# Kernel optimization log

Hardware: AMD Instinct MI355X
Metric: run time of the kernel (lower is better)

## Reference

```python
import math
import jax, jax.numpy as jnp
import numpy as np

D = 512
MEM_LEN = 1024
RATIO = 2


def setup_inputs() -> dict:
    key = jax.random.key(0)
    ks = jax.random.split(key, 16)
    s = 1.0 / math.sqrt(D)
    inp = {
        "x": jax.random.normal(ks[0], (4, 2048, D), jnp.float32),
        "fine_mem": jax.random.normal(ks[1], (8, 256, D), jnp.float32),
        "cmem_seq": jax.random.normal(ks[2], (16, 128, D), jnp.float32),
        "comp_query": jax.random.normal(ks[3], (D,), jnp.float32) * 0.02,
        "comp_W": jax.random.normal(ks[4], (D, D), jnp.float32) * s,
        "comp_b": jnp.zeros((D,), jnp.float32),
        "k_W": jax.random.normal(ks[5], (D, D), jnp.float32) * s,
        "k_b": jnp.zeros((D,), jnp.float32),
        "v_W": jax.random.normal(ks[6], (D, D), jnp.float32) * s,
        "v_b": jnp.zeros((D,), jnp.float32),
        "xk_W": jax.random.normal(ks[7], (D, D), jnp.float32) * s,
        "xk_b": jnp.zeros((D,), jnp.float32),
        "ck_W": jax.random.normal(ks[8], (D, D), jnp.float32) * s,
        "ck_b": jnp.zeros((D,), jnp.float32),
        "cv_W": jax.random.normal(ks[9], (D, D), jnp.float32) * s,
        "cv_b": jnp.zeros((D,), jnp.float32),
    }
    return inp


def _compress(combined, comp_query, comp_W, comp_b):
    # AttentionPoolCompressor, vectorized: L tokens -> L//RATIO pooled tokens
    L, d = combined.shape
    L_out = max(L // RATIO, 1)
    c = combined.reshape(L_out, RATIO, d)                      # [L_out, r, d]
    logits = jnp.einsum("d,lrd->lr", comp_query, c) * (d ** -0.5)
    w = jax.nn.softmax(logits, axis=-1)
    pooled = jnp.einsum("lr,lrd->ld", w, c)                    # [L_out, d]
    return pooled @ comp_W + comp_b


def _interp_linear(comp, L):
    # F.interpolate(mode='linear', align_corners=False) along length dim
    L_out = comp.shape[0]
    i = jnp.arange(L, dtype=jnp.float32)
    src = jnp.clip((i + 0.5) * (L_out / L) - 0.5, 0.0, L_out - 1)
    i0 = jnp.floor(src).astype(jnp.int32)
    i1 = jnp.minimum(i0 + 1, L_out - 1)
    frac = (src - i0)[:, None]
    return (1.0 - frac) * comp[i0] + frac * comp[i1]


def reference(x, fine_mem, cmem_seq, comp_query, comp_W, comp_b,
              k_W, k_b, v_W, v_b, xk_W, xk_b, ck_W, ck_b, cv_W, cv_b):
    B, S, d = x.shape
    Nf, Lm, _ = fine_mem.shape
    scale = d ** -0.5

    # keys/values over the ORIGINAL memories (projections precede eviction)
    fine_k = fine_mem @ k_W + k_b      # [Nf, Lm, d]
    fine_v = fine_mem @ v_W + v_b
    cmem_k = cmem_seq @ ck_W + ck_b    # [Nc, Lc, d]
    cmem_v = cmem_seq @ cv_W + cv_b

    # eviction: take leading chunks until cumsum >= mem_len/2 (static)
    K = min(int(math.ceil(0.5 * MEM_LEN / Lm)), Nf)
    combined = fine_mem[:K].reshape(K * Lm, d)                 # [L, d]
    compressed = _compress(combined, comp_query, comp_W, comp_b)
    decoded = _interp_linear(compressed, combined.shape[0])
    recon_loss = jnp.mean((decoded - combined) ** 2)

    # cross-attention over concatenated memory
    query = x @ xk_W + xk_b                                    # [B, S, d]
    mem_k = jnp.concatenate([fine_k.reshape(-1, d), cmem_k.reshape(-1, d)], 0)
    mem_v = jnp.concatenate([fine_v.reshape(-1, d), cmem_v.reshape(-1, d)], 0)
    scores = jnp.einsum("bsd,md->bsm", query, mem_k) * scale   # [B, S, M]
    attn = jax.nn.softmax(scores, axis=-1)
    mem_out = jnp.einsum("bsm,md->bsd", attn, mem_v)
    output = x + mem_out
    return (output, recon_loss)
```

## Files before the change

kernel.cpp:

```cpp
#include <hip/hip_runtime.h>

typedef __attribute__((ext_vector_type(8))) short bf16x8;
typedef __attribute__((ext_vector_type(4))) float f32x4;

#define MFMA16(a,b,c) __builtin_amdgcn_mfma_f32_16x16x32_bf16((a),(b),(c),0,0,0)

__device__ __forceinline__ unsigned short f2bf(float f) {
  unsigned int u = __builtin_bit_cast(unsigned int, f);
  u = (u + 0x7FFFu + ((u >> 16) & 1u)) >> 16;
  return (unsigned short)u;
}
__device__ __forceinline__ float bf2f(unsigned short u) {
  unsigned int v = ((unsigned int)u) << 16;
  return __builtin_bit_cast(float, v);
}
__device__ __forceinline__ unsigned int pack_bf16(float a, float b) {
  return ((unsigned int)f2bf(b) << 16) | (unsigned int)f2bf(a);
}

__global__ __launch_bounds__(256) void cvt_bf16_all(
    const float* __restrict__ x, const float* __restrict__ fine,
    const float* __restrict__ cmem, unsigned short* __restrict__ abf)
{
  size_t off = ((size_t)blockIdx.x * 256 + threadIdx.x) * 4;
  const float* src;
  if (off < (size_t)8192*512)        src = x + off;
  else if (off < (size_t)10240*512)  src = fine + (off - (size_t)8192*512);
  else                               src = cmem + (off - (size_t)10240*512);
  float4 v = *(const float4*)src;
  unsigned long long pk = (unsigned long long)f2bf(v.x)
    | ((unsigned long long)f2bf(v.y) << 16)
    | ((unsigned long long)f2bf(v.z) << 32)
    | ((unsigned long long)f2bf(v.w) << 48);
  *(unsigned long long*)(abf + off) = pk;
}

__global__ __launch_bounds__(256) void wt_transpose5(
    const float* __restrict__ W0, const float* __restrict__ W1,
    const float* __restrict__ W2, const float* __restrict__ W3,
    const float* __restrict__ W4,
    unsigned short* __restrict__ O0, unsigned short* __restrict__ O1,
    unsigned short* __restrict__ O2, unsigned short* __restrict__ O3,
    unsigned short* __restrict__ O4)
{
  const float* W; unsigned short* Wt;
  switch (blockIdx.z) {
    case 0: W = W0; Wt = O0; break;
    case 1: W = W1; Wt = O1; break;
    case 2: W = W2; Wt = O2; break;
    case 3: W = W3; Wt = O3; break;
    default: W = W4; Wt = O4; break;
  }
  __shared__ unsigned short T[32][33];
  int kb = blockIdx.x * 32, nb = blockIdx.y * 32;
  int tx = threadIdx.x & 31, ty = threadIdx.x >> 5;
  #pragma unroll
  for (int s = 0; s < 4; ++s)
    T[ty + 8*s][tx] = f2bf(W[(kb + ty + 8*s)*512 + nb + tx]);
  __syncthreads();
  #pragma unroll
  for (int s = 0; s < 4; ++s)
    Wt[(nb + ty + 8*s)*512 + kb + tx] = T[tx][ty + 8*s];
}

__global__ __launch_bounds__(256) void v_transpose(const unsigned short* __restrict__ V,
    unsigned short* __restrict__ Vt)
{
  __shared__ unsigned short T[32][33];
  int mb = blockIdx.x * 32, db = blockIdx.y * 32;
  int tx = threadIdx.x & 31, ty = threadIdx.x >> 5;
  #pragma unroll
  for (int s = 0; s < 4; ++s)
    T[ty + 8*s][tx] = V[(mb + ty + 8*s)*512 + db + tx];
  __syncthreads();
  #pragma unroll
  for (int s = 0; s < 4; ++s)
    Vt[(db + ty + 8*s)*4096 + mb + tx] = T[tx][ty + 8*s];
}

__global__ __launch_bounds__(256) void proj_all(
    const unsigned short* __restrict__ abf,
    const unsigned short* __restrict__ WtXK, const unsigned short* __restrict__ WtK,
    const unsigned short* __restrict__ WtV,  const unsigned short* __restrict__ WtCK,
    const unsigned short* __restrict__ WtCV,
    const float* __restrict__ xkb, const float* __restrict__ kb2, const float* __restrict__ vb2,
    const float* __restrict__ ckb, const float* __restrict__ cvb,
    unsigned short* __restrict__ qry, unsigned short* __restrict__ memk,
    unsigned short* __restrict__ memv)
{
  const unsigned short* A; const unsigned short* Bt; const float* bias; unsigned short* C;
  int m0;
  int bx = blockIdx.x;
  if (bx < 64) { A = abf; Bt = WtXK; bias = xkb; C = qry; m0 = bx * 128; }
  else {
    int seg = (bx - 64) >> 4;
    m0 = ((bx - 64) & 15) * 128;
    switch (seg) {
      case 0:  A = abf + (size_t)8192*512;  Bt = WtK;  bias = kb2; C = memk;            break;
      case 1:  A = abf + (size_t)10240*512; Bt = WtCK; bias = ckb; C = memk + 2048*512; break;
      case 2:  A = abf + (size_t)8192*512;  Bt = WtV;  bias = vb2; C = memv;            break;
      default: A = abf + (size_t)10240*512; Bt = WtCV; bias = cvb; C = memv + 2048*512; break;
    }
  }
  const float cs = (bx < 64) ? 0.04419417382415922f : 1.0f;

  __shared__ unsigned short As[128*32];
  __shared__ unsigned short Bs[64*32];
  const int tid = threadIdx.x;
  const int w = tid >> 6, lane = tid & 63;
  const int lr = lane & 15, lg = lane >> 4;
  const int wm = w >> 1, wn = w & 1;
  const int n0 = blockIdx.y * 64;

  f32x4 acc[4][2];
  #pragma unroll
  for (int mt = 0; mt < 4; ++mt)
    #pragma unroll
    for (int nt = 0; nt < 2; ++nt) acc[mt][nt] = (f32x4){0.f,0.f,0.f,0.f};

  const int arow = lane >> 2;
  const int acol = (lane & 3) * 8;

  for (int kb = 0; kb < 512; kb += 32) {
    #pragma unroll
    for (int j = 0; j < 2; ++j) {
      int r0 = (w*2 + j) * 16;
      __builtin_amdgcn_global_load_lds(
        (const __attribute__((address_space(1))) unsigned int*)
          (A + (size_t)(m0 + r0 + arow)*512 + kb + acol),
        (__attribute__((address_space(3))) unsigned int*)(&As[r0*32]), 16, 0, 0);
    }
    {
      int r0 = w * 16;
      __builtin_amdgcn_global_load_lds(
        (const __attribute__((address_space(1))) unsigned int*)
          (Bt + (size_t)(n0 + r0 + arow)*512 + kb + acol),
        (__attribute__((address_space(3))) unsigned int*)(&Bs[r0*32]), 16, 0, 0);
    }
    __syncthreads();
    bf16x8 af[4], bfr[2];
    #pragma unroll
    for (int mt = 0; mt < 4; ++mt)
      af[mt] = *(const bf16x8*)&As[(wm*64 + mt*16 + lr)*32 + lg*8];
    #pragma unroll
    for (int nt = 0; nt < 2; ++nt)
      bfr[nt] = *(const bf16x8*)&Bs[(wn*32 + nt*16 + lr)*32 + lg*8];
    #pragma unroll
    for (int mt = 0; mt < 4; ++mt)
      #pragma unroll
      for (int nt = 0; nt < 2; ++nt)
        acc[mt][nt] = MFMA16(af[mt], bfr[nt], acc[mt][nt]);
    __syncthreads();
  }
  #pragma unroll
  for (int nt = 0; nt < 2; ++nt) {
    int col = n0 + wn*32 + nt*16 + lr;
    float bv = bias[col];
    #pragma unroll
    for (int mt = 0; mt < 4; ++mt) {
      #pragma unroll
      for (int j = 0; j < 4; ++j) {
        int row = m0 + wm*64 + mt*16 + lg*4 + j;
        C[row*512 + col] = f2bf((acc[mt][nt][j] + bv) * cs);
      }
    }
  }
}

template<int NC>
__global__ __launch_bounds__(256, 2) void attn_kernel(
    const unsigned short* __restrict__ q,
    const unsigned short* __restrict__ mk,
    const unsigned short* __restrict__ vt,
    unsigned short* __restrict__ opart,
    float* __restrict__ mpart,
    float* __restrict__ lpart)
{
  constexpr int CK = 4096 / NC;
  constexpr int ITERS = CK / 64;
  constexpr int PLW = 68;

  __shared__ unsigned short Ks[64*520];
  __shared__ unsigned short Pl[64*PLW];
  __shared__ float Fl[64];
  __shared__ unsigned int Tf[4];

  const int tid = threadIdx.x;
  const int w = tid >> 6, lane = tid & 63;
  const int lr = lane & 15, lg = lane >> 4;
  const int bid = blockIdx.x;
  const int chunk = bid & (NC - 1);
  const int qb = bid / NC;
  const int q0blk = qb * 64;
  const int kvbase = chunk * CK;

  const unsigned short* qgp = q + (size_t)(q0blk + w*16 + lr) * 512 + lg*8;

  f32x4 o[32];
  #pragma unroll
  for (int nt = 0; nt < 32; ++nt) o[nt] = (f32x4){0.f,0.f,0.f,0.f};
  float m = -1e30f, l = 0.f;

  const unsigned short* vgp = vt + (size_t)(w*128 + lr) * 4096 + kvbase + lg*8;

  #define STAGE_K(IT) do {                                                        \
    int kv0_ = kvbase + (IT) * 64;                                                \
    _Pragma("unroll")                                                             \
    for (int i_ = 0; i_ < 16; ++i_) {                                             \
      int r_ = w * 16 + i_;                                                       \
      __builtin_amdgcn_global_load_lds(                                           \
        (const __attribute__((address_space(1))) unsigned int*)                   \
          (mk + (kv0_ + r_)*512 + lane*8),                                        \
        (__attribute__((address_space(3))) unsigned int*)(&Ks[r_*520]), 16, 0, 0);\
    }                                                                             \
  } while (0)

  STAGE_K(0);
  __syncthreads();

  const unsigned short* kp = &Ks[lr * 520];

  for (int it = 0; it < ITERS; ++it) {
    f32x4 t0 = (f32x4){0.f,0.f,0.f,0.f}, t1 = (f32x4){0.f,0.f,0.f,0.f};
    f32x4 t2 = (f32x4){0.f,0.f,0.f,0.f}, t3 = (f32x4){0.f,0.f,0.f,0.f};
    __builtin_amdgcn_s_setprio(1);
    #pragma unroll
    for (int ks = 0; ks < 16; ++ks) {
      bf16x8 qf  = *(const bf16x8*)(qgp + ks*32);
      bf16x8 kb0 = *(const bf16x8*)(kp + ks*32 + lg*8);
      bf16x8 kb1 = *(const bf16x8*)(kp + 16*520 + ks*32 + lg*8);
      bf16x8 kb2 = *(const bf16x8*)(kp + 32*520 + ks*32 + lg*8);
      bf16x8 kb3 = *(const bf16x8*)(kp + 48*520 + ks*32 + lg*8);
      t0 = MFMA16(kb0, qf, t0);
      t1 = MFMA16(kb1, qf, t1);
      t2 = MFMA16(kb2, qf, t2);
      t3 = MFMA16(kb3, qf, t3);
    }
    __builtin_amdgcn_s_setprio(0);

    float pm = fmaxf(fmaxf(fmaxf(t0[0], t0[1]), fmaxf(t0[2], t0[3])),
                     fmaxf(fmaxf(t1[0], t1[1]), fmaxf(t1[2], t1[3])));
    pm = fmaxf(pm, fmaxf(fmaxf(fmaxf(t2[0], t2[1]), fmaxf(t2[2], t2[3])),
                         fmaxf(fmaxf(t3[0], t3[1]), fmaxf(t3[2], t3[3]))));
    pm = fmaxf(pm, __shfl_xor(pm, 16));
    pm = fmaxf(pm, __shfl_xor(pm, 32));

    bool trig = !__all(pm <= m + 8.f);
    if (trig) {
      float mn = fmaxf(m, pm);
      float fl = __expf(m - mn);
      l *= fl;
      m = mn;
      if (lg == 0) Fl[w*16 + lr] = fl;
    }
    if (lane == 0) Tf[w] = trig ? 1u : 0u;

    float p0[4], p1[4], p2[4], p3[4];
    #pragma unroll
    for (int j = 0; j < 4; ++j) {
      p0[j] = __expf(t0[j] - m);
      p1[j] = __expf(t1[j] - m);
      p2[j] = __expf(t2[j] - m);
      p3[j] = __expf(t3[j] - m);
    }
    float rs = ((p0[0]+p0[1]) + (p0[2]+p0[3])) + ((p1[0]+p1[1]) + (p1[2]+p1[3]))
             + ((p2[0]+p2[1]) + (p2[2]+p2[3])) + ((p3[0]+p3[1]) + (p3[2]+p3[3]));
    rs += __shfl_xor(rs, 16);
    rs += __shfl_xor(rs, 32);
    l += rs;

    {
      unsigned short* pr = &Pl[(w*16 + lr)*PLW + lg*4];
      *(uint2*)(pr)      = make_uint2(pack_bf16(p0[0], p0[1]), pack_bf16(p0[2], p0[3]));
      *(uint2*)(pr + 16) = make_uint2(pack_bf16(p1[0], p1[1]), pack_bf16(p1[2], p1[3]));
      *(uint2*)(pr + 32) = make_uint2(pack_bf16(p2[0], p2[1]), pack_bf16(p2[2], p2[3]));
      *(uint2*)(pr + 48) = make_uint2(pack_bf16(p3[0], p3[1]), pack_bf16(p3[2], p3[3]));
    }
    __syncthreads();

    if (it + 1 < ITERS) STAGE_K(it + 1);

    unsigned int tf0 = Tf[0], tf1 = Tf[1], tf2 = Tf[2], tf3 = Tf[3];
    if (tf0 | tf1 | tf2 | tf3) {
      #pragma unroll
      for (int qt = 0; qt < 4; ++qt) {
        unsigned int tfq = (qt == 0) ? tf0 : (qt == 1) ? tf1 : (qt == 2) ? tf2 : tf3;
        if (tfq) {
          f32x4 fq = *(const f32x4*)&Fl[qt*16 + lg*4];
          #pragma unroll
          for (int dt = 0; dt < 8; ++dt) {
            o[qt*8 + dt][0] *= fq[0]; o[qt*8 + dt][1] *= fq[1];
            o[qt*8 + dt][2] *= fq[2]; o[qt*8 + dt][3] *= fq[3];
          }
        }
      }
    }

    const unsigned short* vit = vgp + it*64;
    #pragma unroll
    for (int kvh = 0; kvh < 2; ++kvh) {
      bf16x8 pa[4];
      #pragma unroll
      for (int qt = 0; qt < 4; ++qt)
        pa[qt] = *(const bf16x8*)&Pl[(qt*16 + lr)*PLW + kvh*32 + lg*8];
      #pragma unroll
      for (int dh = 0; dh < 2; ++dh) {
        bf16x8 vb[4];
        #pragma unroll
        for (int dt = 0; dt < 4; ++dt)
          vb[dt] = *(const bf16x8*)(vit + kvh*32 + (size_t)(dh*4 + dt)*16*4096);
        __builtin_amdgcn_s_setprio(1);
        #pragma unroll
        for (int qt = 0; qt < 4; ++qt) {
          #pragma unroll
          for (int dt = 0; dt < 4; ++dt)
            o[qt*8 + dh*4 + dt] = MFMA16(pa[qt], vb[dt], o[qt*8 + dh*4 + dt]);
        }
        __builtin_amdgcn_s_setprio(0);
      }
    }
    __syncthreads();
  }

  unsigned short* ob = opart + (size_t)chunk * 8192 * 512;
  #pragma unroll
  for (int qt = 0; qt < 4; ++qt) {
    #pragma unroll
    for (int dt = 0; dt < 8; ++dt) {
      #pragma unroll
      for (int j = 0; j < 4; ++j) {
        int row = q0blk + qt*16 + lg*4 + j;
        int col = w*128 + dt*16 + lr;
        ob[row*512 + col] = f2bf(o[qt*8 + dt][j]);
      }
    }
  }
  if (lane < 16) {
    mpart[chunk*8192 + q0blk + w*16 + lane] = m;
    lpart[chunk*8192 + q0blk + w*16 + lane] = l;
  }
  #undef STAGE_K
}

template<int NC>
__global__ __launch_bounds__(256) void attn_combine(
    const unsigned short* __restrict__ opart, const float* __restrict__ mpart,
    const float* __restrict__ lpart, const float* __restrict__ x,
    float* __restrict__ out)
{
  int row = blockIdx.x * 4 + (threadIdx.x >> 6);
  int t = threadIdx.x & 63;
  int d0 = t * 8;
  float mc[NC], lc[NC];
  #pragma unroll
  for (int c = 0; c < NC; ++c) { mc[c] = mpart[c*8192 + row]; lc[c] = lpart[c*8192 + row]; }
  float M = mc[0];
  #pragma unroll
  for (int c = 1; c < NC; ++c) M = fmaxf(M, mc[c]);
  float wc[NC], denom = 0.f;
  #pragma unroll
  for (int c = 0; c < NC; ++c) { wc[c] = __expf(mc[c] - M); denom += wc[c] * lc[c]; }
  float inv = 1.0f / denom;
  float acc[8] = {0.f,0.f,0.f,0.f,0.f,0.f,0.f,0.f};
  const unsigned short* base = opart + (size_t)row*512 + d0;
  #pragma unroll
  for (int c = 0; c < NC; ++c) {
    int4 v = *(const int4*)(base + (size_t)c * 8192 * 512);
    const unsigned short* u = (const unsigned short*)&v;
    #pragma unroll
    for (int e = 0; e < 8; ++e) acc[e] += wc[c] * bf2f(u[e]);
  }
  float4 xv0 = *(const float4*)(x + row*512 + d0);
  float4 xv1 = *(const float4*)(x + row*512 + d0 + 4);
  float4 o0, o1;
  o0.x = xv0.x + acc[0]*inv; o0.y = xv0.y + acc[1]*inv;
  o0.z = xv0.z + acc[2]*inv; o0.w = xv0.w + acc[3]*inv;
  o1.x = xv1.x + acc[4]*inv; o1.y = xv1.y + acc[5]*inv;
  o1.z = xv1.z + acc[6]*inv; o1.w = xv1.w + acc[7]*inv;
  *(float4*)(out + row*512 + d0)     = o0;
  *(float4*)(out + row*512 + d0 + 4) = o1;
}

__global__ __launch_bounds__(256) void compress_pool(const float* __restrict__ fine,
    const float* __restrict__ cq, float* __restrict__ pooled, float* __restrict__ loss)
{
  if (blockIdx.x == 0 && threadIdx.x == 0) *loss = 0.f;
  int l = blockIdx.x;
  int t = threadIdx.x;
  const float* c0 = fine + (2*l)*512;
  const float* c1 = c0 + 512;
  float q0 = cq[t], q1 = cq[t+256];
  float a0 = q0*c0[t] + q1*c0[t+256];
  float a1 = q0*c1[t] + q1*c1[t+256];
  #pragma unroll
  for (int m = 1; m < 64; m <<= 1) { a0 += __shfl_xor(a0, m); a1 += __shfl_xor(a1, m); }
  __shared__ float r0[4], r1[4];
  int w = t >> 6;
  if ((t & 63) == 0) { r0[w] = a0; r1[w] = a1; }
  __syncthreads();
  const float sc = 0.04419417382415922f;
  float g0 = (r0[0]+r0[1]+r0[2]+r0[3]) * sc;
  float g1 = (r1[0]+r1[1]+r1[2]+r1[3]) * sc;
  float mx = fmaxf(g0, g1);
  float e0 = __expf(g0-mx), e1 = __expf(g1-mx);
  float inv = 1.0f/(e0+e1);
  float w0 = e0*inv, w1 = e1*inv;
  pooled[l*512 + t]       = w0*c0[t]     + w1*c1[t];
  pooled[l*512 + t + 256] = w0*c0[t+256] + w1*c1[t+256];
}

__global__ __launch_bounds__(256) void comp_gemm(const float* __restrict__ P,
    const float* __restrict__ W, const float* __restrict__ b, float* __restrict__ out)
{
  int gid = blockIdx.x * 256 + threadIdx.x;
  int m = gid >> 9, n = gid & 511;
  const float* a = P + m * 512;
  float acc = b[n];
  #pragma unroll 8
  for (int k = 0; k < 512; ++k) acc += a[k] * W[k*512 + n];
  out[gid] = acc;
}

__global__ __launch_bounds__(256) void interp_loss(const float* __restrict__ comp,
    const float* __restrict__ fine, float* __restrict__ loss)
{
  float acc = 0.f;
  #pragma unroll
  for (int s = 0; s < 4; ++s) {
    int e = blockIdx.x*1024 + s*256 + threadIdx.x;
    int i = e >> 9, d = e & 511;
    float src = fminf(fmaxf((i + 0.5f)*0.5f - 0.5f, 0.f), 255.f);
    int i0 = (int)src;
    int i1 = min(i0 + 1, 255);
    float fr = src - (float)i0;
    float dec = (1.f - fr)*comp[i0*512 + d] + fr*comp[i1*512 + d];
    float df = dec - fine[e];
    acc += df*df;
  }
  #pragma unroll
  for (int m = 1; m < 64; m <<= 1) acc += __shfl_xor(acc, m);
  __shared__ float r[4];
  int w = threadIdx.x >> 6;
  if ((threadIdx.x & 63) == 0) r[w] = acc;
  __syncthreads();
  if (threadIdx.x == 0)
    atomicAdd(loss, (r[0]+r[1]+r[2]+r[3]) * (1.0f/262144.0f));
}

extern "C" void kernel_launch(void* const* d_in, const int* in_sizes, int n_in,
                              void* d_out, int out_size, void* d_ws, size_t ws_size,
                              hipStream_t stream) {
  const float* x     = (const float*)d_in[0];
  const float* fine  = (const float*)d_in[1];
  const float* cmem  = (const float*)d_in[2];
  const float* cq    = (const float*)d_in[3];
  const float* compW = (const float*)d_in[4];
  const float* compb = (const float*)d_in[5];
  const float* kW    = (const float*)d_in[6];
  const float* kb_   = (const float*)d_in[7];
  const float* vW    = (const float*)d_in[8];
  const float* vb_   = (const float*)d_in[9];
  const float* xkW   = (const float*)d_in[10];
  const float* xkb   = (const float*)d_in[11];
  const float* ckW   = (const float*)d_in[12];
  const float* ckb   = (const float*)d_in[13];
  const float* cvW   = (const float*)d_in[14];
  const float* cvb   = (const float*)d_in[15];

  char* ws = (char*)d_ws;
  const size_t WT = 512*512*2;
  unsigned short* WtK  = (unsigned short*)(ws + 0*WT);
  unsigned short* WtV  = (unsigned short*)(ws + 1*WT);
  unsigned short* WtCK = (unsigned short*)(ws + 2*WT);
  unsigned short* WtCV = (unsigned short*)(ws + 3*WT);
  unsigned short* WtXK = (unsigned short*)(ws + 4*WT);
  char* base = ws + 5*WT;
  unsigned short* memk = (unsigned short*)(base);
  unsigned short* memv = (unsigned short*)(base + (4u<<20));
  unsigned short* vt   = (unsigned short*)(base + (8u<<20));
  unsigned short* qry  = (unsigned short*)(base + (12u<<20));
  float* pooled        = (float*)(base + (20u<<20));
  float* comp          = (float*)(base + (20u<<20) + (512u<<10));
  unsigned short* opart= (unsigned short*)(base + (21u<<20));
  float* mpart         = (float*)(base + (21u<<20) + (32ull<<20));
  float* lpart         = mpart + 4*8192;
  unsigned short* abf  = (unsigned short*)(base + (54u<<20));

  float* out  = (float*)d_out;
  float* loss = out + 8192*512;

  cvt_bf16_all<<<6144, 256, 0, stream>>>(x, fine, cmem, abf);

  wt_transpose5<<<dim3(16,16,5), 256, 0, stream>>>(kW, vW, ckW, cvW, xkW,
                                                   WtK, WtV, WtCK, WtCV, WtXK);

  proj_all<<<dim3(128,8), 256, 0, stream>>>(abf,
      WtXK, WtK, WtV, WtCK, WtCV,
      xkb, kb_, vb_, ckb, cvb,
      qry, memk, memv);

  v_transpose<<<dim3(128,16), 256, 0, stream>>>(memv, vt);

  attn_kernel<4><<<512, 256, 0, stream>>>(qry, memk, vt, opart, mpart, lpart);
  attn_combine<4><<<2048, 256, 0, stream>>>(opart, mpart, lpart, x, out);

  compress_pool<<<256, 256, 0, stream>>>(fine, cq, pooled, loss);
  comp_gemm<<<512, 256, 0, stream>>>(pooled, compW, compb, comp);
  interp_loss<<<256, 256, 0, stream>>>(comp, fine, loss);
}
```

Measured before the change: 186.7 us.

## Merge independent kernels into fewer launches and drop setprio in attention

Groups the original nine launches into five. Bf16 conversion, weight transposes and compress pooling now share one prep kernel. The projection GEMM and compression GEMM share one kernel, and the V transpose and interp-loss share a post kernel, with each branch picked by block index. The goal is to cut launch overhead and let the small recon-loss work overlap with the big stages instead of running serially at the end. It also removes the s_setprio hints around the MFMA loops in the attention kernel, which may change wave scheduling.

```diff
diff --git a/kernel.cpp b/kernel.cpp
--- a/kernel.cpp
+++ b/kernel.cpp
@@ -18,67 +18,80 @@
   return ((unsigned int)f2bf(b) << 16) | (unsigned int)f2bf(a);
 }
 
-__global__ __launch_bounds__(256) void cvt_bf16_all(
+__global__ __launch_bounds__(256) void prep_kernel(
     const float* __restrict__ x, const float* __restrict__ fine,
-    const float* __restrict__ cmem, unsigned short* __restrict__ abf)
-{
-  size_t off = ((size_t)blockIdx.x * 256 + threadIdx.x) * 4;
-  const float* src;
-  if (off < (size_t)8192*512)        src = x + off;
-  else if (off < (size_t)10240*512)  src = fine + (off - (size_t)8192*512);
-  else                               src = cmem + (off - (size_t)10240*512);
-  float4 v = *(const float4*)src;
-  unsigned long long pk = (unsigned long long)f2bf(v.x)
-    | ((unsigned long long)f2bf(v.y) << 16)
-    | ((unsigned long long)f2bf(v.z) << 32)
-    | ((unsigned long long)f2bf(v.w) << 48);
-  *(unsigned long long*)(abf + off) = pk;
-}
-
-__global__ __launch_bounds__(256) void wt_transpose5(
+    const float* __restrict__ cmem, unsigned short* __restrict__ abf,
     const float* __restrict__ W0, const float* __restrict__ W1,
     const float* __restrict__ W2, const float* __restrict__ W3,
     const float* __restrict__ W4,
     unsigned short* __restrict__ O0, unsigned short* __restrict__ O1,
     unsigned short* __restrict__ O2, unsigned short* __restrict__ O3,
-    unsigned short* __restrict__ O4)
-{
-  const float* W; unsigned short* Wt;
-  switch (blockIdx.z) {
-    case 0: W = W0; Wt = O0; break;
-    case 1: W = W1; Wt = O1; break;
-    case 2: W = W2; Wt = O2; break;
-    case 3: W = W3; Wt = O3; break;
-    default: W = W4; Wt = O4; break;
-  }
-  __shared__ unsigned short T[32][33];
-  int kb = blockIdx.x * 32, nb = blockIdx.y * 32;
-  int tx = threadIdx.x & 31, ty = threadIdx.x >> 5;
-  #pragma unroll
-  for (int s = 0; s < 4; ++s)
-    T[ty + 8*s][tx] = f2bf(W[(kb + ty + 8*s)*512 + nb + tx]);
-  __syncthreads();
-  #pragma unroll
-  for (int s = 0; s < 4; ++s)
-    Wt[(nb + ty + 8*s)*512 + kb + tx] = T[tx][ty + 8*s];
-}
-
-__global__ __launch_bounds__(256) void v_transpose(const unsigned short* __restrict__ V,
-    unsigned short* __restrict__ Vt)
+    unsigned short* __restrict__ O4,
+    const float* __restrict__ cq, float* __restrict__ pooled, float* __restrict__ loss)
 {
   __shared__ unsigned short T[32][33];
-  int mb = blockIdx.x * 32, db = blockIdx.y * 32;
-  int tx = threadIdx.x & 31, ty = threadIdx.x >> 5;
-  #pragma unroll
-  for (int s = 0; s < 4; ++s)
-    T[ty + 8*s][tx] = V[(mb + ty + 8*s)*512 + db + tx];
-  __syncthreads();
-  #pragma unroll
-  for (int s = 0; s < 4; ++s)
-    Vt[(db + ty + 8*s)*4096 + mb + tx] = T[tx][ty + 8*s];
-}
-
-__global__ __launch_bounds__(256) void proj_all(
+  __shared__ float r0s[4], r1s[4];
+  int bx = blockIdx.x;
+  int tid = threadIdx.x;
+
+  if (bx < 6144) {
+    size_t off = ((size_t)bx * 256 + tid) * 4;
+    const float* src;
+    if (off < (size_t)8192*512)        src = x + off;
+    else if (off < (size_t)10240*512)  src = fine + (off - (size_t)8192*512);
+    else                               src = cmem + (off - (size_t)10240*512);
+    float4 v = *(const float4*)src;
+    unsigned long long pk = (unsigned long long)f2bf(v.x)
+      | ((unsigned long long)f2bf(v.y) << 16)
+      | ((unsigned long long)f2bf(v.z) << 32)
+      | ((unsigned long long)f2bf(v.w) << 48);
+    *(unsigned long long*)(abf + off) = pk;
+  } else if (bx < 7424) {
+    int idx = bx - 6144;
+    int z = idx >> 8, rem = idx & 255;
+    int kb = (rem & 15) * 32, nb = (rem >> 4) * 32;
+    const float* W; unsigned short* Wt;
+    switch (z) {
+      case 0: W = W0; Wt = O0; break;
+      case 1: W = W1; Wt = O1; break;
+      case 2: W = W2; Wt = O2; break;
+      case 3: W = W3; Wt = O3; break;
+      default: W = W4; Wt = O4; break;
+    }
+    int tx = tid & 31, ty = tid >> 5;
+    #pragma unroll
+    for (int s = 0; s < 4; ++s)
+      T[ty + 8*s][tx] = f2bf(W[(kb + ty + 8*s)*512 + nb + tx]);
+    __syncthreads();
+    #pragma unroll
+    for (int s = 0; s < 4; ++s)
+      Wt[(nb + ty + 8*s)*512 + kb + tx] = T[tx][ty + 8*s];
+  } else {
+    int l = bx - 7424;
+    if (l == 0 && tid == 0) *loss = 0.f;
+    const float* c0 = fine + (2*l)*512;
+    const float* c1 = c0 + 512;
+    float q0 = cq[tid], q1 = cq[tid+256];
+    float a0 = q0*c0[tid] + q1*c0[tid+256];
+    float a1 = q0*c1[tid] + q1*c1[tid+256];
+    #pragma unroll
+    for (int mm = 1; mm < 64; mm <<= 1) { a0 += __shfl_xor(a0, mm); a1 += __shfl_xor(a1, mm); }
+    int w = tid >> 6;
+    if ((tid & 63) == 0) { r0s[w] = a0; r1s[w] = a1; }
+    __syncthreads();
+    const float sc = 0.04419417382415922f;
+    float g0 = (r0s[0]+r0s[1]+r0s[2]+r0s[3]) * sc;
+    float g1 = (r1s[0]+r1s[1]+r1s[2]+r1s[3]) * sc;
+    float mx = fmaxf(g0, g1);
+    float e0 = __expf(g0-mx), e1 = __expf(g1-mx);
+    float inv = 1.0f/(e0+e1);
+    float w0 = e0*inv, w1 = e1*inv;
+    pooled[l*512 + tid]       = w0*c0[tid]     + w1*c1[tid];
+    pooled[l*512 + tid + 256] = w0*c0[tid+256] + w1*c1[tid+256];
+  }
+}
+
+__global__ __launch_bounds__(256) void gemm_kernel(
     const unsigned short* __restrict__ abf,
     const unsigned short* __restrict__ WtXK, const unsigned short* __restrict__ WtK,
     const unsigned short* __restrict__ WtV,  const unsigned short* __restrict__ WtCK,
@@ -86,11 +99,30 @@
     const float* __restrict__ xkb, const float* __restrict__ kb2, const float* __restrict__ vb2,
     const float* __restrict__ ckb, const float* __restrict__ cvb,
     unsigned short* __restrict__ qry, unsigned short* __restrict__ memk,
-    unsigned short* __restrict__ memv)
+    unsigned short* __restrict__ memv,
+    const float* __restrict__ P, const float* __restrict__ compW,
+    const float* __restrict__ compb, float* __restrict__ comp)
 {
+  __shared__ unsigned short As[128*32];
+  __shared__ unsigned short Bs[64*32];
+  const int tid = threadIdx.x;
+  int bxg = blockIdx.x;
+
+  if (bxg >= 1024) {
+    int gid = (bxg - 1024) * 256 + tid;
+    int m = gid >> 9, n = gid & 511;
+    const float* a = P + m * 512;
+    float acc = compb[n];
+    #pragma unroll 8
+    for (int k = 0; k < 512; ++k) acc += a[k] * compW[k*512 + n];
+    comp[gid] = acc;
+    return;
+  }
+
+  int bx = bxg >> 3;
+  int n0 = (bxg & 7) * 64;
   const unsigned short* A; const unsigned short* Bt; const float* bias; unsigned short* C;
   int m0;
-  int bx = blockIdx.x;
   if (bx < 64) { A = abf; Bt = WtXK; bias = xkb; C = qry; m0 = bx * 128; }
   else {
     int seg = (bx - 64) >> 4;
@@ -104,13 +136,9 @@
   }
   const float cs = (bx < 64) ? 0.04419417382415922f : 1.0f;
 
-  __shared__ unsigned short As[128*32];
-  __shared__ unsigned short Bs[64*32];
-  const int tid = threadIdx.x;
   const int w = tid >> 6, lane = tid & 63;
   const int lr = lane & 15, lg = lane >> 4;
   const int wm = w >> 1, wn = w & 1;
-  const int n0 = blockIdx.y * 64;
 
   f32x4 acc[4][2];
   #pragma unroll
@@ -164,6 +192,51 @@
         C[row*512 + col] = f2bf((acc[mt][nt][j] + bv) * cs);
       }
     }
+  }
+}
+
+__global__ __launch_bounds__(256) void post_kernel(
+    const unsigned short* __restrict__ V, unsigned short* __restrict__ Vt,
+    const float* __restrict__ comp, const float* __restrict__ fine,
+    float* __restrict__ loss)
+{
+  __shared__ unsigned short T[32][33];
+  __shared__ float r[4];
+  int bx = blockIdx.x;
+  int tid = threadIdx.x;
+
+  if (bx < 2048) {
+    int mb = (bx & 127) * 32, db = (bx >> 7) * 32;
+    int tx = tid & 31, ty = tid >> 5;
+    #pragma unroll
+    for (int s = 0; s < 4; ++s)
+      T[ty + 8*s][tx] = V[(mb + ty + 8*s)*512 + db + tx];
+    __syncthreads();
+    #pragma unroll
+    for (int s = 0; s < 4; ++s)
+      Vt[(db + ty + 8*s)*4096 + mb + tx] = T[tx][ty + 8*s];
+  } else {
+    int bid = bx - 2048;
+    float acc = 0.f;
+    #pragma unroll
+    for (int s = 0; s < 4; ++s) {
+      int e = bid*1024 + s*256 + tid;
+      int i = e >> 9, d = e & 511;
+      float src = fminf(fmaxf((i + 0.5f)*0.5f - 0.5f, 0.f), 255.f);
+      int i0 = (int)src;
+      int i1 = min(i0 + 1, 255);
+      float fr = src - (float)i0;
+      float dec = (1.f - fr)*comp[i0*512 + d] + fr*comp[i1*512 + d];
+      float df = dec - fine[e];
+      acc += df*df;
+    }
+    #pragma unroll
+    for (int mm = 1; mm < 64; mm <<= 1) acc += __shfl_xor(acc, mm);
+    int w = tid >> 6;
+    if ((tid & 63) == 0) r[w] = acc;
+    __syncthreads();
+    if (tid == 0)
+      atomicAdd(loss, (r[0]+r[1]+r[2]+r[3]) * (1.0f/262144.0f));
   }
 }
 
@@ -223,7 +296,6 @@
   for (int it = 0; it < ITERS; ++it) {
     f32x4 t0 = (f32x4){0.f,0.f,0.f,0.f}, t1 = (f32x4){0.f,0.f,0.f,0.f};
     f32x4 t2 = (f32x4){0.f,0.f,0.f,0.f}, t3 = (f32x4){0.f,0.f,0.f,0.f};
-    __builtin_amdgcn_s_setprio(1);
     #pragma unroll
     for (int ks = 0; ks < 16; ++ks) {
       bf16x8 qf  = *(const bf16x8*)(qgp + ks*32);
@@ -236,7 +308,6 @@
       t2 = MFMA16(kb2, qf, t2);
       t3 = MFMA16(kb3, qf, t3);
     }
-    __builtin_amdgcn_s_setprio(0);
 
     float pm = fmaxf(fmaxf(fmaxf(t0[0], t0[1]), fmaxf(t0[2], t0[3])),
                      fmaxf(fmaxf(t1[0], t1[1]), fmaxf(t1[2], t1[3])));
@@ -309,14 +380,12 @@
         #pragma unroll
         for (int dt = 0; dt < 4; ++dt)
           vb[dt] = *(const bf16x8*)(vit + kvh*32 + (size_t)(dh*4 + dt)*16*4096);
-        __builtin_amdgcn_s_setprio(1);
         #pragma unroll
         for (int qt = 0; qt < 4; ++qt) {
           #pragma unroll
           for (int dt = 0; dt < 4; ++dt)
             o[qt*8 + dh*4 + dt] = MFMA16(pa[qt], vb[dt], o[qt*8 + dh*4 + dt]);
         }
-        __builtin_amdgcn_s_setprio(0);
       }
     }
     __syncthreads();
@@ -379,72 +448,6 @@
   o1.z = xv1.z + acc[6]*inv; o1.w = xv1.w + acc[7]*inv;
   *(float4*)(out + row*512 + d0)     = o0;
   *(float4*)(out + row*512 + d0 + 4) = o1;
-}
-
-__global__ __launch_bounds__(256) void compress_pool(const float* __restrict__ fine,
-    const float* __restrict__ cq, float* __restrict__ pooled, float* __restrict__ loss)
-{
-  if (blockIdx.x == 0 && threadIdx.x == 0) *loss = 0.f;
-  int l = blockIdx.x;
-  int t = threadIdx.x;
-  const float* c0 = fine + (2*l)*512;
-  const float* c1 = c0 + 512;
-  float q0 = cq[t], q1 = cq[t+256];
-  float a0 = q0*c0[t] + q1*c0[t+256];
-  float a1 = q0*c1[t] + q1*c1[t+256];
-  #pragma unroll
-  for (int m = 1; m < 64; m <<= 1) { a0 += __shfl_xor(a0, m); a1 += __shfl_xor(a1, m); }
-  __shared__ float r0[4], r1[4];
-  int w = t >> 6;
-  if ((t & 63) == 0) { r0[w] = a0; r1[w] = a1; }
-  __syncthreads();
-  const float sc = 0.04419417382415922f;
-  float g0 = (r0[0]+r0[1]+r0[2]+r0[3]) * sc;
-  float g1 = (r1[0]+r1[1]+r1[2]+r1[3]) * sc;
-  float mx = fmaxf(g0, g1);
-  float e0 = __expf(g0-mx), e1 = __expf(g1-mx);
-  float inv = 1.0f/(e0+e1);
-  float w0 = e0*inv, w1 = e1*inv;
-  pooled[l*512 + t]       = w0*c0[t]     + w1*c1[t];
-  pooled[l*512 + t + 256] = w0*c0[t+256] + w1*c1[t+256];
-}
-
-__global__ __launch_bounds__(256) void comp_gemm(const float* __restrict__ P,
-    const float* __restrict__ W, const float* __restrict__ b, float* __restrict__ out)
-{
-  int gid = blockIdx.x * 256 + threadIdx.x;
-  int m = gid >> 9, n = gid & 511;
-  const float* a = P + m * 512;
-  float acc = b[n];
-  #pragma unroll 8
-  for (int k = 0; k < 512; ++k) acc += a[k] * W[k*512 + n];
-  out[gid] = acc;
-}
-
-__global__ __launch_bounds__(256) void interp_loss(const float* __restrict__ comp,
-    const float* __restrict__ fine, float* __restrict__ loss)
-{
-  float acc = 0.f;
-  #pragma unroll
-  for (int s = 0; s < 4; ++s) {
-    int e = blockIdx.x*1024 + s*256 + threadIdx.x;
-    int i = e >> 9, d = e & 511;
-    float src = fminf(fmaxf((i + 0.5f)*0.5f - 0.5f, 0.f), 255.f);
-    int i0 = (int)src;
-    int i1 = min(i0 + 1, 255);
-    float fr = src - (float)i0;
-    float dec = (1.f - fr)*comp[i0*512 + d] + fr*comp[i1*512 + d];
-    float df = dec - fine[e];
-    acc += df*df;
-  }
-  #pragma unroll
-  for (int m = 1; m < 64; m <<= 1) acc += __shfl_xor(acc, m);
-  __shared__ float r[4];
-  int w = threadIdx.x >> 6;
-  if ((threadIdx.x & 63) == 0) r[w] = acc;
-  __syncthreads();
-  if (threadIdx.x == 0)
-    atomicAdd(loss, (r[0]+r[1]+r[2]+r[3]) * (1.0f/262144.0f));
 }
 
 extern "C" void kernel_launch(void* const* d_in, const int* in_sizes, int n_in,
@@ -489,22 +492,18 @@
   float* out  = (float*)d_out;
   float* loss = out + 8192*512;
 
-  cvt_bf16_all<<<6144, 256, 0, stream>>>(x, fine, cmem, abf);
-
-  wt_transpose5<<<dim3(16,16,5), 256, 0, stream>>>(kW, vW, ckW, cvW, xkW,
-                                                   WtK, WtV, WtCK, WtCV, WtXK);
-
-  proj_all<<<dim3(128,8), 256, 0, stream>>>(abf,
+  prep_kernel<<<7680, 256, 0, stream>>>(x, fine, cmem, abf,
+      kW, vW, ckW, cvW, xkW, WtK, WtV, WtCK, WtCV, WtXK,
+      cq, pooled, loss);
+
+  gemm_kernel<<<1536, 256, 0, stream>>>(abf,
       WtXK, WtK, WtV, WtCK, WtCV,
       xkb, kb_, vb_, ckb, cvb,
-      qry, memk, memv);
-
-  v_transpose<<<dim3(128,16), 256, 0, stream>>>(memv, vt);
+      qry, memk, memv,
+      pooled, compW, compb, comp);
+
+  post_kernel<<<2304, 256, 0, stream>>>(memv, vt, comp, fine, loss);
 
   attn_kernel<4><<<512, 256, 0, stream>>>(qry, memk, vt, opart, mpart, lpart);
   attn_combine<4><<<2048, 256, 0, stream>>>(opart, mpart, lpart, x, out);
-
-  compress_pool<<<256, 256, 0, stream>>>(fine, cq, pooled, loss);
-  comp_gemm<<<512, 256, 0, stream>>>(pooled, compW, compb, comp);
-  interp_loss<<<256, 256, 0, stream>>>(comp, fine, loss);
-}
+}
```

New measurement: 180.7 us. 1.03x faster.
